# Kernel optimization log

Hardware: AMD Instinct MI355X
Metric: run time of the kernel (lower is better)

## Reference

```python
import jax, jax.numpy as jnp
import numpy as np

B, S, C = 4, 2048, 2048
D = C // 4  # head dim = 512

def setup_inputs() -> dict:
    key = jax.random.key(0)
    k1, k2, k3, k4, k5 = jax.random.split(key, 5)
    scale = 1.0 / np.sqrt(C)
    return {
        "x": jax.random.normal(k1, (B, S, C), dtype=jnp.float32),
        "Wqkv": jax.random.normal(k2, (3 * D, C), dtype=jnp.float32) * scale,
        "bqkv": jax.random.normal(k3, (3 * D,), dtype=jnp.float32) * 0.01,
        "Wo": jax.random.normal(k4, (C, D), dtype=jnp.float32) * (1.0 / np.sqrt(D)),
        "bo": jax.random.normal(k5, (C,), dtype=jnp.float32) * 0.01,
    }

def reference(x, Wqkv, bqkv, Wo, bo):
    Bx, Sx, Cx = x.shape
    d = Cx // 4
    # fused QKV projection: [B,S,3d] -> split into q,k,v each [B,S,d]
    qkv = jnp.einsum('bsc,oc->bso', x, Wqkv) + bqkv
    qkv = qkv.reshape(Bx, Sx, 3, d)
    q, k, v = qkv[:, :, 0], qkv[:, :, 1], qkv[:, :, 2]
    # scaled dot-product attention (full [B,S,S] scores, as in original)
    attn = jnp.einsum('bqd,bkd->bqk', q, k) / jnp.sqrt(jnp.asarray(d, x.dtype))
    attn = jax.nn.softmax(attn, axis=-1)
    ctx = jnp.einsum('bqk,bkd->bqd', attn, v)
    # output projection d -> C
    return jnp.einsum('bsd,od->bso', ctx, Wo) + bo
```

## Files before the change

kernel.cpp:

```cpp
#include <hip/hip_runtime.h>
#include <math.h>


typedef __bf16 bf16;
typedef bf16 bf16x8 __attribute__((ext_vector_type(8)));
typedef bf16 bf16x4 __attribute__((ext_vector_type(4)));
typedef float f32x4 __attribute__((ext_vector_type(4)));

#define BB 4
#define SS 2048
#define CC 2048
#define DD 512
#define ND3 1536
#define MM 8192

typedef const __attribute__((address_space(1))) unsigned int g_u32;
typedef __attribute__((address_space(3))) unsigned int l_u32;

__device__ __forceinline__ void gl_lds16(const bf16* g, bf16* l) {
    __builtin_amdgcn_global_load_lds((g_u32*)g, (l_u32*)l, 16, 0, 0);
}

#define VMW(n) asm volatile("s_waitcnt vmcnt(" #n ")" ::: "memory")
#define BAR    __builtin_amdgcn_s_barrier()

#define N4_X   (MM * CC / 4)
#define N4_WQ  (ND3 * CC / 4)
#define N4_WO  (CC * DD / 4)
#define N4_RS  (MM / 4)
#define N4_TOT (N4_X + N4_WQ + N4_WO + N4_RS)

__global__ __launch_bounds__(256) void prep(const float* __restrict__ x,
                                            const float* __restrict__ Wqkv,
                                            const float* __restrict__ Wo,
                                            bf16* __restrict__ xb,
                                            bf16* __restrict__ wqkvb,
                                            bf16* __restrict__ wob,
                                            float* __restrict__ rsum) {
    int i = blockIdx.x * 256 + threadIdx.x;
    const int stride = gridDim.x * 256;
    for (; i < N4_TOT; i += stride) {
        if (i < N4_X + N4_WQ + N4_WO) {
            const float* src; bf16* dst; int j = i;
            if (j < N4_X)                { src = x;    dst = xb; }
            else if (j < N4_X + N4_WQ)   { src = Wqkv; dst = wqkvb; j -= N4_X; }
            else                         { src = Wo;   dst = wob;   j -= N4_X + N4_WQ; }
            float4 v = ((const float4*)src)[j];
            bf16x4 o;
            o[0] = (bf16)v.x; o[1] = (bf16)v.y; o[2] = (bf16)v.z; o[3] = (bf16)v.w;
            ((bf16x4*)dst)[j] = o;
        } else {
            int j = i - (N4_X + N4_WQ + N4_WO);
            ((float4*)rsum)[j] = float4{0.f, 0.f, 0.f, 0.f};
        }
    }
}

#define SLOT_E 16384
#define CH_B   8192

template <bool OUT_BF16, int EPI>
__device__ __forceinline__ void gemm256_body(const bf16* __restrict__ A,
                                             const bf16* __restrict__ Bm,
                                             const float* __restrict__ bias,
                                             float* __restrict__ rowsum,
                                             bf16* __restrict__ vTp,
                                             void* __restrict__ Cv,
                                             int K, int lda, int ldb, int ldc,
                                             long ab, long bb, long cb,
                                             float scale) {
    extern __shared__ bf16 lds[];
    A  += (size_t)blockIdx.z * ab;
    Bm += (size_t)blockIdx.z * bb;
    const int m0 = blockIdx.y * 256, n0 = blockIdx.x * 256;
    const int t = threadIdx.x, lane = t & 63, w = t >> 6;
    const int wm = (w >> 2) * 128, wn = (w & 3) * 64;
    const int cl = lane & 15, q = lane >> 4;
    const int swzr = (q ^ ((cl >> 1) & 3)) * 8;
    const int srow = t >> 2;
    const int swz  = (t & 3) ^ ((t >> 3) & 3);
    const bf16* pa = A  + (size_t)(m0 + srow) * lda + swz * 8;
    const bf16* pb = Bm + (size_t)(n0 + srow) * ldb + swz * 8;
    bf16* lw = lds + w * 512;

    f32x4 acc[8][4] = {};
    const int NC = K >> 5;

    auto STAGE = [&](int j) {
        bf16* s = lw + (j & 3) * SLOT_E;
        const bf16* ga = pa + j * 32;
        const bf16* gb = pb + j * 32;
        gl_lds16(ga,                     s);
        gl_lds16(ga + (size_t)128 * lda, s + 4096);
        gl_lds16(gb,                     s + CH_B);
        gl_lds16(gb + (size_t)128 * ldb, s + CH_B + 4096);
    };
    auto FRAGS = [&](int j, bf16x8 (&af)[8], bf16x8 (&bfr)[4]) {
        const bf16* sa = lds + (j & 3) * SLOT_E + (wm + cl) * 32 + swzr;
        const bf16* sb = lds + (j & 3) * SLOT_E + CH_B + (wn + cl) * 32 + swzr;
#pragma unroll
        for (int i = 0; i < 8; i++)  af[i]  = *(const bf16x8*)(sa + i * 512);
#pragma unroll
        for (int jj = 0; jj < 4; jj++) bfr[jj] = *(const bf16x8*)(sb + jj * 512);
    };
    auto MFMAS = [&](bf16x8 (&af)[8], bf16x8 (&bfr)[4]) {
        __builtin_amdgcn_s_setprio(1);
#pragma unroll
        for (int i = 0; i < 8; i++)
#pragma unroll
            for (int jj = 0; jj < 4; jj++)
                acc[i][jj] = __builtin_amdgcn_mfma_f32_16x16x32_bf16(
                                 af[i], bfr[jj], acc[i][jj], 0, 0, 0);
        __builtin_amdgcn_s_setprio(0);
    };

    STAGE(0); STAGE(1); STAGE(2);
    VMW(8); BAR;

    for (int j = 0; j < NC - 3; ++j) {
        bf16x8 af[8], bfr[4];
        FRAGS(j, af, bfr);
        STAGE(j + 3);
        MFMAS(af, bfr);
        VMW(8); BAR;
    }
    {   bf16x8 af[8], bfr[4];
        FRAGS(NC - 3, af, bfr); MFMAS(af, bfr);
        VMW(4); BAR;
    }
    {   bf16x8 af[8], bfr[4];
        FRAGS(NC - 2, af, bfr); MFMAS(af, bfr);
        VMW(0); BAR;
    }
    {   bf16x8 af[8], bfr[4];
        FRAGS(NC - 1, af, bfr); MFMAS(af, bfr);
    }

    if constexpr (EPI == 7) {
#pragma unroll
        for (int i = 0; i < 8; i++) {
            float ex[4][4];
#pragma unroll
            for (int jj = 0; jj < 4; jj++)
#pragma unroll
                for (int r = 0; r < 4; r++)
                    ex[jj][r] = __expf(acc[i][jj][r] * scale);
#pragma unroll
            for (int jj = 0; jj < 4; jj++) {
                int col = n0 + wn + jj * 16 + cl;
#pragma unroll
                for (int r = 0; r < 4; r++) {
                    int row = m0 + wm + i * 16 + q * 4 + r;
                    ((bf16*)Cv)[(size_t)blockIdx.z * cb + (size_t)row * ldc + col] =
                        (bf16)ex[jj][r];
                }
            }
#pragma unroll
            for (int r = 0; r < 4; r++) {
                float rs = ex[0][r] + ex[1][r] + ex[2][r] + ex[3][r];
                rs += __shfl_xor(rs, 1, 64);
                rs += __shfl_xor(rs, 2, 64);
                rs += __shfl_xor(rs, 4, 64);
                rs += __shfl_xor(rs, 8, 64);
                if (cl == 0) {
                    int row = m0 + wm + i * 16 + q * 4 + r;
                    atomicAdd(&rowsum[(size_t)blockIdx.z * SS + row], rs);
                }
            }
        }
        return;
    }

    const bool v_block = (EPI == 3) && (n0 >= 1024);
#pragma unroll
    for (int i = 0; i < 8; i++) {
#pragma unroll
        for (int jj = 0; jj < 4; jj++) {
            int col = n0 + wn + jj * 16 + cl;
            float bvv = bias ? bias[col] : 0.0f;
            if (v_block) {
                int row = m0 + wm + i * 16 + q * 4;
                int b = row >> 11, s = row & 2047;
                bf16x4 o;
#pragma unroll
                for (int r = 0; r < 4; r++) o[r] = (bf16)(acc[i][jj][r] * scale + bvv);
                *(bf16x4*)&vTp[((size_t)b * DD + (col - 1024)) * SS + s] = o;
            } else {
#pragma unroll
                for (int r = 0; r < 4; r++) {
                    int row = m0 + wm + i * 16 + q * 4 + r;
                    float val = acc[i][jj][r] * scale + bvv;
                    if (OUT_BF16)
                        ((bf16*)Cv)[(size_t)blockIdx.z * cb + (size_t)row * ldc + col] = (bf16)val;
                    else
                        ((float*)Cv)[(size_t)blockIdx.z * cb + (size_t)row * ldc + col] = val;
                }
            }
        }
    }
}

__global__ __launch_bounds__(256) void k_pv(const bf16* __restrict__ A,
        const bf16* __restrict__ Bm, float* __restrict__ rowsum,
        bf16* __restrict__ Cv, int K, int lda, int ldb, int ldc,
        long ab, long bb, long cb) {
    __shared__ bf16 As[128 * 64];
    __shared__ bf16 Bs[128 * 64];
    A += (size_t)blockIdx.z * ab;
    Bm += (size_t)blockIdx.z * bb;
    const int m0 = blockIdx.y * 128, n0 = blockIdx.x * 128;
    const int t = threadIdx.x, lane = t & 63, w = t >> 6;
    const int wm = (w >> 1) * 64, wn = (w & 1) * 64;
    const int q = lane >> 4, cl = lane & 15;
    const int srow = lane >> 3;
    const int sblk = (lane & 7) ^ srow;
    const int scol = sblk * 8;
    const bf16* pa = A + (size_t)(m0 + w * 32 + srow) * lda + scol;
    const bf16* pb = Bm + (size_t)(n0 + w * 32 + srow) * ldb + scol;
    bf16* lA = As + (w * 32) * 64;
    bf16* lB = Bs + (w * 32) * 64;
    const int rblk0 = (q ^ (cl & 7)) * 8;
    const int rblk1 = ((4 + q) ^ (cl & 7)) * 8;

    f32x4 acc[4][4] = {};
    for (int k0 = 0; k0 < K; k0 += 64) {
#pragma unroll
        for (int n = 0; n < 4; n++)
            gl_lds16(pa + k0 + (size_t)(n * 8) * lda, lA + n * 8 * 64);
#pragma unroll
        for (int n = 0; n < 4; n++)
            gl_lds16(pb + k0 + (size_t)(n * 8) * ldb, lB + n * 8 * 64);
        __syncthreads();
#pragma unroll
        for (int h = 0; h < 2; h++) {
            const int rb = h ? rblk1 : rblk0;
            bf16x8 af[4], bfr[4];
#pragma unroll
            for (int i = 0; i < 4; i++)
                af[i] = *(const bf16x8*)&As[(wm + i * 16 + cl) * 64 + rb];
#pragma unroll
            for (int j = 0; j < 4; j++)
                bfr[j] = *(const bf16x8*)&Bs[(wn + j * 16 + cl) * 64 + rb];
#pragma unroll
            for (int i = 0; i < 4; i++)
#pragma unroll
                for (int j = 0; j < 4; j++)
                    acc[i][j] = __builtin_amdgcn_mfma_f32_16x16x32_bf16(af[i], bfr[j], acc[i][j], 0, 0, 0);
        }
        __syncthreads();
    }

    float inv[4][4];
#pragma unroll
    for (int i = 0; i < 4; i++)
#pragma unroll
        for (int r = 0; r < 4; r++)
            inv[i][r] = 1.0f / rowsum[(size_t)blockIdx.z * SS + m0 + wm + i * 16 + q * 4 + r];
#pragma unroll
    for (int i = 0; i < 4; i++)
#pragma unroll
        for (int j = 0; j < 4; j++) {
            int col = n0 + wn + j * 16 + cl;
#pragma unroll
            for (int r = 0; r < 4; r++) {
                int row = m0 + wm + i * 16 + q * 4 + r;
                Cv[(size_t)blockIdx.z * cb + (size_t)row * ldc + col] =
                    (bf16)(acc[i][j][r] * inv[i][r]);
            }
        }
}

__global__ __launch_bounds__(512, 2) void k_qkv(const bf16* A, const bf16* Bm,
        const float* bias, bf16* vTp, void* Cv, int K, int lda, int ldb, int ldc,
        float scale) {
    gemm256_body<true, 3>(A, Bm, bias, nullptr, vTp, Cv, K, lda, ldb, ldc, 0, 0, 0, scale);
}
__global__ __launch_bounds__(512, 2) void k_score(const bf16* A, const bf16* Bm,
        float* rowsum, void* Cv, int K, int lda, int ldb, int ldc,
        long ab, long bb, long cb, float scale) {
    gemm256_body<true, 7>(A, Bm, nullptr, rowsum, nullptr, Cv, K, lda, ldb, ldc, ab, bb, cb, scale);
}
__global__ __launch_bounds__(512, 2) void k_out(const bf16* A, const bf16* Bm,
        const float* bias, void* Cv, int K, int lda, int ldb, int ldc,
        float scale) {
    gemm256_body<false, 0>(A, Bm, bias, nullptr, nullptr, Cv, K, lda, ldb, ldc, 0, 0, 0, scale);
}

extern "C" void kernel_launch(void* const* d_in, const int* in_sizes, int n_in,
                              void* d_out, int out_size, void* d_ws, size_t ws_size,
                              hipStream_t stream) {
    const float* x    = (const float*)d_in[0];
    const float* Wqkv = (const float*)d_in[1];
    const float* bqkv = (const float*)d_in[2];
    const float* Wo   = (const float*)d_in[3];
    const float* bo   = (const float*)d_in[4];
    float* out = (float*)d_out;

    char* ws = (char*)d_ws;
    size_t off = 0;
    bf16* xb    = (bf16*)(ws + off); off += (size_t)MM * CC * 2;
    bf16* wqkvb = (bf16*)(ws + off); off += (size_t)ND3 * CC * 2;
    bf16* wob   = (bf16*)(ws + off); off += (size_t)CC * DD * 2;
    bf16* qkvb  = (bf16*)(ws + off); off += (size_t)MM * ND3 * 2;
    bf16* vT    = (bf16*)(ws + off); off += (size_t)BB * DD * SS * 2;
    bf16* expS  = (bf16*)(ws + off); off += (size_t)BB * SS * SS * 2;
    bf16* ctxb  = (bf16*)(ws + off); off += (size_t)MM * DD * 2;
    float* rsum = (float*)(ws + off); off += (size_t)MM * 4;

    static int lds_attr_set = 0;
    if (!lds_attr_set) {
        hipFuncSetAttribute((const void*)k_qkv,
                            hipFuncAttributeMaxDynamicSharedMemorySize, 131072);
        hipFuncSetAttribute((const void*)k_score,
                            hipFuncAttributeMaxDynamicSharedMemorySize, 131072);
        hipFuncSetAttribute((const void*)k_out,
                            hipFuncAttributeMaxDynamicSharedMemorySize, 131072);
        lds_attr_set = 1;
    }

    prep<<<2048, 256, 0, stream>>>(x, Wqkv, Wo, xb, wqkvb, wob, rsum);

    k_qkv<<<dim3(ND3 / 256, MM / 256, 1), 512, 131072, stream>>>(
        xb, wqkvb, bqkv, vT, qkvb, CC, CC, CC, ND3, 1.0f);

    k_score<<<dim3(SS / 256, SS / 256, BB), 512, 131072, stream>>>(
        qkvb , qkvb + 512 , rsum, expS,
        DD, ND3, ND3, SS,
        (long)SS * ND3, (long)SS * ND3, (long)SS * SS,
        0.044194173824159216f );

    k_pv<<<dim3(DD / 128, SS / 128, BB), 256, 0, stream>>>(
        expS, vT, rsum, ctxb,
        SS, SS, SS, DD,
        (long)SS * SS, (long)DD * SS, (long)SS * DD);

    k_out<<<dim3(CC / 256, MM / 256, 1), 512, 131072, stream>>>(
        ctxb, wob, bo, out, DD, DD, DD, CC, 1.0f);

    (void)in_sizes; (void)n_in; (void)out_size; (void)ws_size;
}
```

Measured before the change: 294.3 us.

## Double-buffer GEMM LDS, transpose score tile for vector stores, shrink PV tile

The shared GEMM body drops from four LDS pipeline slots to two, halving dynamic LDS to 64 KB. Staging now happens after an lgkm wait and barrier instead of being overlapped with the fragment loads. The score kernel swaps its operands so it computes K·Qᵀ and writes the exp tile transposed with packed bf16x4 stores. Its row-sum reduction becomes a column reduction with fewer atomics. The PV kernel uses 128x64 tiles, doubling the grid for more parallelism. Together these trade prefetch depth for occupancy and aim to cut store and atomic traffic.

After: 297.0 us. About the same (+0.9%).

```diff
diff --git a/kernel.cpp b/kernel.cpp
--- a/kernel.cpp
+++ b/kernel.cpp
@@ -22,6 +22,7 @@
 }
 
 #define VMW(n) asm volatile("s_waitcnt vmcnt(" #n ")" ::: "memory")
+#define LKW0   asm volatile("s_waitcnt lgkmcnt(0)" ::: "memory")
 #define BAR    __builtin_amdgcn_s_barrier()
 
 #define N4_X   (MM * CC / 4)
@@ -87,7 +88,7 @@
     const int NC = K >> 5;
 
     auto STAGE = [&](int j) {
-        bf16* s = lw + (j & 3) * SLOT_E;
+        bf16* s = lw + (j & 1) * SLOT_E;
         const bf16* ga = pa + j * 32;
         const bf16* gb = pb + j * 32;
         gl_lds16(ga,                     s);
@@ -96,8 +97,8 @@
         gl_lds16(gb + (size_t)128 * ldb, s + CH_B + 4096);
     };
     auto FRAGS = [&](int j, bf16x8 (&af)[8], bf16x8 (&bfr)[4]) {
-        const bf16* sa = lds + (j & 3) * SLOT_E + (wm + cl) * 32 + swzr;
-        const bf16* sb = lds + (j & 3) * SLOT_E + CH_B + (wn + cl) * 32 + swzr;
+        const bf16* sa = lds + (j & 1) * SLOT_E + (wm + cl) * 32 + swzr;
+        const bf16* sb = lds + (j & 1) * SLOT_E + CH_B + (wn + cl) * 32 + swzr;
 #pragma unroll
         for (int i = 0; i < 8; i++)  af[i]  = *(const bf16x8*)(sa + i * 512);
 #pragma unroll
@@ -114,18 +115,15 @@
         __builtin_amdgcn_s_setprio(0);
     };
 
-    STAGE(0); STAGE(1); STAGE(2);
-    VMW(8); BAR;
-
-    for (int j = 0; j < NC - 3; ++j) {
+    STAGE(0); STAGE(1);
+    VMW(4); BAR;
+
+    for (int j = 0; j < NC - 2; ++j) {
         bf16x8 af[8], bfr[4];
         FRAGS(j, af, bfr);
-        STAGE(j + 3);
         MFMAS(af, bfr);
-        VMW(8); BAR;
-    }
-    {   bf16x8 af[8], bfr[4];
-        FRAGS(NC - 3, af, bfr); MFMAS(af, bfr);
+        LKW0; BAR;
+        STAGE(j + 2);
         VMW(4); BAR;
     }
     {   bf16x8 af[8], bfr[4];
@@ -136,37 +134,32 @@
         FRAGS(NC - 1, af, bfr); MFMAS(af, bfr);
     }
 
-    if constexpr (EPI == 7) {
-#pragma unroll
-        for (int i = 0; i < 8; i++) {
-            float ex[4][4];
-#pragma unroll
-            for (int jj = 0; jj < 4; jj++)
-#pragma unroll
-                for (int r = 0; r < 4; r++)
-                    ex[jj][r] = __expf(acc[i][jj][r] * scale);
+    if constexpr (EPI == 4) {
+        float cs[4] = {0.f, 0.f, 0.f, 0.f};
+#pragma unroll
+        for (int i = 0; i < 8; i++)
 #pragma unroll
             for (int jj = 0; jj < 4; jj++) {
                 int col = n0 + wn + jj * 16 + cl;
+                int row = m0 + wm + i * 16 + q * 4;
+                bf16x4 o;
 #pragma unroll
                 for (int r = 0; r < 4; r++) {
-                    int row = m0 + wm + i * 16 + q * 4 + r;
-                    ((bf16*)Cv)[(size_t)blockIdx.z * cb + (size_t)row * ldc + col] =
-                        (bf16)ex[jj][r];
+                    float e = __expf(acc[i][jj][r] * scale);
+                    cs[jj] += e;
+                    o[r] = (bf16)e;
                 }
+                *(bf16x4*)&((bf16*)Cv)[(size_t)blockIdx.z * cb + (size_t)col * ldc + row] = o;
             }
 #pragma unroll
-            for (int r = 0; r < 4; r++) {
-                float rs = ex[0][r] + ex[1][r] + ex[2][r] + ex[3][r];
-                rs += __shfl_xor(rs, 1, 64);
-                rs += __shfl_xor(rs, 2, 64);
-                rs += __shfl_xor(rs, 4, 64);
-                rs += __shfl_xor(rs, 8, 64);
-                if (cl == 0) {
-                    int row = m0 + wm + i * 16 + q * 4 + r;
-                    atomicAdd(&rowsum[(size_t)blockIdx.z * SS + row], rs);
-                }
-            }
+        for (int jj = 0; jj < 4; jj++) {
+            cs[jj] += __shfl_xor(cs[jj], 16, 64);
+            cs[jj] += __shfl_xor(cs[jj], 32, 64);
+        }
+        if (q == 0) {
+#pragma unroll
+            for (int jj = 0; jj < 4; jj++)
+                atomicAdd(&rowsum[(size_t)blockIdx.z * SS + n0 + wn + jj * 16 + cl], cs[jj]);
         }
         return;
     }
@@ -205,44 +198,44 @@
         bf16* __restrict__ Cv, int K, int lda, int ldb, int ldc,
         long ab, long bb, long cb) {
     __shared__ bf16 As[128 * 64];
-    __shared__ bf16 Bs[128 * 64];
+    __shared__ bf16 Bs[64 * 64];
     A += (size_t)blockIdx.z * ab;
     Bm += (size_t)blockIdx.z * bb;
-    const int m0 = blockIdx.y * 128, n0 = blockIdx.x * 128;
+    const int m0 = blockIdx.y * 128, n0 = blockIdx.x * 64;
     const int t = threadIdx.x, lane = t & 63, w = t >> 6;
-    const int wm = (w >> 1) * 64, wn = (w & 1) * 64;
+    const int wm = w * 32;
     const int q = lane >> 4, cl = lane & 15;
     const int srow = lane >> 3;
     const int sblk = (lane & 7) ^ srow;
     const int scol = sblk * 8;
     const bf16* pa = A + (size_t)(m0 + w * 32 + srow) * lda + scol;
-    const bf16* pb = Bm + (size_t)(n0 + w * 32 + srow) * ldb + scol;
+    const bf16* pb = Bm + (size_t)(n0 + w * 16 + srow) * ldb + scol;
     bf16* lA = As + (w * 32) * 64;
-    bf16* lB = Bs + (w * 32) * 64;
+    bf16* lB = Bs + (w * 16) * 64;
     const int rblk0 = (q ^ (cl & 7)) * 8;
     const int rblk1 = ((4 + q) ^ (cl & 7)) * 8;
 
-    f32x4 acc[4][4] = {};
+    f32x4 acc[2][4] = {};
     for (int k0 = 0; k0 < K; k0 += 64) {
 #pragma unroll
         for (int n = 0; n < 4; n++)
             gl_lds16(pa + k0 + (size_t)(n * 8) * lda, lA + n * 8 * 64);
 #pragma unroll
-        for (int n = 0; n < 4; n++)
+        for (int n = 0; n < 2; n++)
             gl_lds16(pb + k0 + (size_t)(n * 8) * ldb, lB + n * 8 * 64);
         __syncthreads();
 #pragma unroll
         for (int h = 0; h < 2; h++) {
             const int rb = h ? rblk1 : rblk0;
-            bf16x8 af[4], bfr[4];
-#pragma unroll
-            for (int i = 0; i < 4; i++)
+            bf16x8 af[2], bfr[4];
+#pragma unroll
+            for (int i = 0; i < 2; i++)
                 af[i] = *(const bf16x8*)&As[(wm + i * 16 + cl) * 64 + rb];
 #pragma unroll
             for (int j = 0; j < 4; j++)
-                bfr[j] = *(const bf16x8*)&Bs[(wn + j * 16 + cl) * 64 + rb];
-#pragma unroll
-            for (int i = 0; i < 4; i++)
+                bfr[j] = *(const bf16x8*)&Bs[(j * 16 + cl) * 64 + rb];
+#pragma unroll
+            for (int i = 0; i < 2; i++)
 #pragma unroll
                 for (int j = 0; j < 4; j++)
                     acc[i][j] = __builtin_amdgcn_mfma_f32_16x16x32_bf16(af[i], bfr[j], acc[i][j], 0, 0, 0);
@@ -250,17 +243,17 @@
         __syncthreads();
     }
 
-    float inv[4][4];
-#pragma unroll
-    for (int i = 0; i < 4; i++)
+    float inv[2][4];
+#pragma unroll
+    for (int i = 0; i < 2; i++)
 #pragma unroll
         for (int r = 0; r < 4; r++)
             inv[i][r] = 1.0f / rowsum[(size_t)blockIdx.z * SS + m0 + wm + i * 16 + q * 4 + r];
 #pragma unroll
-    for (int i = 0; i < 4; i++)
+    for (int i = 0; i < 2; i++)
 #pragma unroll
         for (int j = 0; j < 4; j++) {
-            int col = n0 + wn + j * 16 + cl;
+            int col = n0 + j * 16 + cl;
 #pragma unroll
             for (int r = 0; r < 4; r++) {
                 int row = m0 + wm + i * 16 + q * 4 + r;
@@ -278,7 +271,7 @@
 __global__ __launch_bounds__(512, 2) void k_score(const bf16* A, const bf16* Bm,
         float* rowsum, void* Cv, int K, int lda, int ldb, int ldc,
         long ab, long bb, long cb, float scale) {
-    gemm256_body<true, 7>(A, Bm, nullptr, rowsum, nullptr, Cv, K, lda, ldb, ldc, ab, bb, cb, scale);
+    gemm256_body<true, 4>(A, Bm, nullptr, rowsum, nullptr, Cv, K, lda, ldb, ldc, ab, bb, cb, scale);
 }
 __global__ __launch_bounds__(512, 2) void k_out(const bf16* A, const bf16* Bm,
         const float* bias, void* Cv, int K, int lda, int ldb, int ldc,
@@ -310,31 +303,31 @@
     static int lds_attr_set = 0;
     if (!lds_attr_set) {
         hipFuncSetAttribute((const void*)k_qkv,
-                            hipFuncAttributeMaxDynamicSharedMemorySize, 131072);
+                            hipFuncAttributeMaxDynamicSharedMemorySize, 65536);
         hipFuncSetAttribute((const void*)k_score,
-                            hipFuncAttributeMaxDynamicSharedMemorySize, 131072);
+                            hipFuncAttributeMaxDynamicSharedMemorySize, 65536);
         hipFuncSetAttribute((const void*)k_out,
-                            hipFuncAttributeMaxDynamicSharedMemorySize, 131072);
+                            hipFuncAttributeMaxDynamicSharedMemorySize, 65536);
         lds_attr_set = 1;
     }
 
     prep<<<2048, 256, 0, stream>>>(x, Wqkv, Wo, xb, wqkvb, wob, rsum);
 
-    k_qkv<<<dim3(ND3 / 256, MM / 256, 1), 512, 131072, stream>>>(
+    k_qkv<<<dim3(ND3 / 256, MM / 256, 1), 512, 65536, stream>>>(
         xb, wqkvb, bqkv, vT, qkvb, CC, CC, CC, ND3, 1.0f);
 
-    k_score<<<dim3(SS / 256, SS / 256, BB), 512, 131072, stream>>>(
-        qkvb , qkvb + 512 , rsum, expS,
+    k_score<<<dim3(SS / 256, SS / 256, BB), 512, 65536, stream>>>(
+        qkvb + 512 , qkvb , rsum, expS,
         DD, ND3, ND3, SS,
         (long)SS * ND3, (long)SS * ND3, (long)SS * SS,
         0.044194173824159216f );
 
-    k_pv<<<dim3(DD / 128, SS / 128, BB), 256, 0, stream>>>(
+    k_pv<<<dim3(DD / 64, SS / 128, BB), 256, 0, stream>>>(
         expS, vT, rsum, ctxb,
         SS, SS, SS, DD,
         (long)SS * SS, (long)DD * SS, (long)SS * DD);
 
-    k_out<<<dim3(CC / 256, MM / 256, 1), 512, 131072, stream>>>(
+    k_out<<<dim3(CC / 256, MM / 256, 1), 512, 65536, stream>>>(
         ctxb, wob, bo, out, DD, DD, DD, CC, 1.0f);
 
     (void)in_sizes; (void)n_in; (void)out_size; (void)ws_size;
```
